# Performance work log

Measured on AMD Instinct MI355X. Metric: run time of the kernel, lower is better.

## Reference

```python
import jax, jax.numpy as jnp
import numpy as np

N_BOND = 2_000_000
N_ATOM = 100_000
N_STRUCT = 2
THREEBODY_CUTOFF = 0.8


def setup_inputs() -> dict:
    key = jax.random.key(0)
    k1, k2 = jax.random.split(key)
    # bonds grouped (sorted) by source atom, as _compute_threebody assumes
    bond_src = jnp.sort(jax.random.randint(k1, (N_BOND,), 0, N_ATOM))
    bond_length = jax.random.uniform(k2, (N_BOND,), dtype=jnp.float32)
    n_atoms = jnp.full((N_STRUCT,), N_ATOM // N_STRUCT, dtype=jnp.int32)
    return {"bond_src": bond_src, "bond_length": bond_length, "n_atoms": n_atoms}


def reference(bond_src, bond_length, n_atoms):
    """Vectorized equivalent of compute_threebody_indices.

    Returns (bond_indices [T,2] pairs of ORIGINAL bond ids, n_triple_ij [n_bond],
    n_triple_i [n_atom], n_triple_s [n_struct]). Replaces the O(n) Python loops
    with segment-sum (degree count), prefix-sum (CSR offsets) and a flat
    enumeration of ordered within-atom bond pairs (j != k).
    """
    n_bond = bond_src.shape[0]
    n_atom = int(jnp.sum(n_atoms))
    n_struct = n_atoms.shape[0]

    # --- filter bonds by three-body cutoff, remember original bond ids ---
    mask = bond_length <= THREEBODY_CUTOFF
    kept = jnp.nonzero(mask)[0]          # original bond indices of surviving bonds
    src = bond_src[kept]                 # still sorted (subset of a sorted array)

    # --- per-atom bond counts and CSR offsets (parallel histogram + scan) ---
    deg = jax.ops.segment_sum(jnp.ones_like(src), src, num_segments=n_atom)
    bond_offset = jnp.cumsum(deg) - deg  # start of each atom's bond block

    # --- triples per atom / per bond / per structure ---
    n_triple_i = deg * (deg - 1)
    T = int(jnp.sum(n_triple_i))

    # --- enumerate all ordered pairs (j, k), j != k, within each atom block ---
    tri_atom = jnp.repeat(jnp.arange(n_atom), n_triple_i, total_repeat_length=T)
    tri_start = (jnp.cumsum(n_triple_i) - n_triple_i)[tri_atom]
    t = jnp.arange(T) - tri_start        # local triple index in [0, d*(d-1))
    d = deg[tri_atom]                    # d >= 2 wherever triples exist
    j = t // (d - 1)
    kp = t % (d - 1)
    k = kp + (kp >= j).astype(kp.dtype)  # skip k == j, preserving loop order
    b0 = bond_offset[tri_atom] + j       # relative (filtered) bond index
    b1 = bond_offset[tri_atom] + k
    bond_indices = jnp.stack([kept[b0], kept[b1]], axis=1)  # back to ORIGINAL ids

    # angles per ORIGINAL bond: deg(src)-1 for surviving bonds, 0 for filtered
    n_triple_ij = jnp.zeros(n_bond, dtype=deg.dtype).at[kept].set(deg[src] - 1)

    # angles per structure
    struct_id = jnp.repeat(jnp.arange(n_struct), n_atoms, total_repeat_length=n_atom)
    n_triple_s = jax.ops.segment_sum(n_triple_i, struct_id, num_segments=n_struct)

    return bond_indices, n_triple_ij, n_triple_i, n_triple_s
```

## Files before the change

### kernel.cpp

```cpp
#include <hip/hip_runtime.h>


#define CUTOFF 0.8f
#define NATOM_C 100000
#define EPB_A 4096
#define EPB_B 1024
#define EPB_IJ 1024
#define TPB2 2048
#define WIN 64

#define ST_AGG (1ull << 32)
#define ST_PFX (2ull << 32)

__device__ __forceinline__ int block_scan_256(int v, int tid, int* sh, int* bsum) {
    sh[tid] = v;
    __syncthreads();
    #pragma unroll
    for (int off = 1; off < 256; off <<= 1) {
        int x = (tid >= off) ? sh[tid - off] : 0;
        __syncthreads();
        sh[tid] += x;
        __syncthreads();
    }
    *bsum = sh[255];
    return sh[tid] - v;
}

__device__ __forceinline__ long long wave_lookback(unsigned long long* status,
                                                   int bid, int bsum, int lane) {
    if (lane == 0)
        __hip_atomic_store(&status[bid],
                           ST_AGG | (unsigned long long)(unsigned)bsum,
                           __ATOMIC_RELEASE, __HIP_MEMORY_SCOPE_AGENT);
    long long excl = 0;
    int w = bid - 1;
    while (w >= 0) {
        int idx = w - lane;
        unsigned long long st;
        if (idx >= 0)
            st = __hip_atomic_load(&status[idx], __ATOMIC_ACQUIRE,
                                   __HIP_MEMORY_SCOPE_AGENT);
        else
            st = ST_PFX;
        unsigned hi = (unsigned)(st >> 32);
        unsigned long long pfx_mask   = __ballot(hi == 2u);
        unsigned long long inval_mask = __ballot(hi != 1u && hi != 2u);
        int first_pfx   = pfx_mask   ? ((int)__ffsll((long long)pfx_mask) - 1)   : 64;
        int first_inval = inval_mask ? ((int)__ffsll((long long)inval_mask) - 1) : 64;
        if (first_inval < first_pfx) continue;
        int val = (lane <= first_pfx) ? (int)(unsigned)st : 0;
        #pragma unroll
        for (int off = 32; off > 0; off >>= 1) val += __shfl_down(val, off, 64);
        val = __shfl(val, 0, 64);
        excl += val;
        if (first_pfx < 64) break;
        w -= 64;
    }
    if (lane == 0)
        __hip_atomic_store(&status[bid],
                           ST_PFX | (unsigned long long)(unsigned)(excl + bsum),
                           __ATOMIC_RELEASE, __HIP_MEMORY_SCOPE_AGENT);
    return excl;
}

__global__ __launch_bounds__(256, 2)
void kA_scan(const float* __restrict__ len, const int* __restrict__ src,
             int* __restrict__ bo, int* __restrict__ ckept,
             unsigned long long* __restrict__ statusA, int n_bond, int n_atom) {
    __shared__ int sh[256];
    __shared__ int sh_last[256];
    __shared__ int sh_bexcl;
    int tid = threadIdx.x;
    int base0 = blockIdx.x * EPB_A + tid * 16;
    int sv[16];
    unsigned mbits = 0;
    #pragma unroll
    for (int g = 0; g < 4; g++) {
        int b = base0 + g * 4;
        if (b + 3 < n_bond) {
            float4 L = *(const float4*)(len + b);
            int4  S = *(const int4*)(src + b);
            sv[g*4+0] = S.x; sv[g*4+1] = S.y; sv[g*4+2] = S.z; sv[g*4+3] = S.w;
            mbits |= (unsigned)(L.x <= CUTOFF) << (g*4+0);
            mbits |= (unsigned)(L.y <= CUTOFF) << (g*4+1);
            mbits |= (unsigned)(L.z <= CUTOFF) << (g*4+2);
            mbits |= (unsigned)(L.w <= CUTOFF) << (g*4+3);
        } else {
            #pragma unroll
            for (int i = 0; i < 4; i++) {
                int idx = b + i;
                bool in = idx < n_bond;
                sv[g*4+i] = in ? src[idx] : 0;
                if (in && len[idx] <= CUTOFF) mbits |= 1u << (g*4+i);
            }
        }
    }
    int s = __popc(mbits);
    sh_last[tid] = sv[15];
    int bsum;
    int texcl = block_scan_256(s, tid, sh, &bsum);
    if (tid < 64) {
        long long e = wave_lookback(statusA, blockIdx.x, bsum, tid);
        if (tid == 0) sh_bexcl = (int)e;
    }
    __syncthreads();
    int run = sh_bexcl + texcl;
    int p;
    if (tid > 0)              p = sh_last[tid - 1];
    else if (blockIdx.x > 0)  p = src[base0 - 1];
    else                      p = -1;
    #pragma unroll
    for (int i = 0; i < 16; i++) {
        int idx = base0 + i;
        if (idx < n_bond) {
            int a = sv[i];
            if (a != p) {
                for (int q = p + 1; q <= a; q++) bo[q] = run;
                p = a;
            }
            if ((mbits >> i) & 1u) { ckept[run] = idx; run++; }
            if (idx == n_bond - 1) {
                for (int q = a + 1; q <= n_atom; q++) bo[q] = run;
            }
        }
    }
}

__global__ __launch_bounds__(256, 2)
void kB_atoms(const int* __restrict__ bo, int* __restrict__ deg,
              int* __restrict__ out_i, int* __restrict__ tstart,
              int* __restrict__ block_atom,
              unsigned long long* __restrict__ statusB, int n_atom) {
    __shared__ int sh[256];
    __shared__ int sh_bexcl;
    int tid = threadIdx.x;
    int base = blockIdx.x * EPB_B + tid * 4;
    int d[4], tr[4];
    if (base + 4 <= n_atom) {
        int4 b4 = *(const int4*)(bo + base);
        int  b5 = bo[base + 4];
        d[0] = b4.y - b4.x; d[1] = b4.z - b4.y; d[2] = b4.w - b4.z; d[3] = b5 - b4.w;
    } else {
        #pragma unroll
        for (int i = 0; i < 4; i++) {
            int a = base + i;
            d[i] = (a < n_atom) ? (bo[a + 1] - bo[a]) : 0;
        }
    }
    int ssum = 0;
    #pragma unroll
    for (int i = 0; i < 4; i++) { tr[i] = d[i] * (d[i] - 1); ssum += tr[i]; }
    #pragma unroll
    for (int i = 0; i < 4; i++) {
        int a = base + i;
        if (a < n_atom) { deg[a] = d[i]; out_i[a] = tr[i]; }
    }
    int bsum;
    int texcl = block_scan_256(ssum, tid, sh, &bsum);
    if (tid < 64) {
        long long e = wave_lookback(statusB, blockIdx.x, bsum, tid);
        if (tid == 0) sh_bexcl = (int)e;
    }
    __syncthreads();
    int run = sh_bexcl + texcl;
    #pragma unroll
    for (int i = 0; i < 4; i++) {
        int a = base + i;
        if (a < n_atom) {
            tstart[a] = run;
            int ts1 = run + tr[i];
            for (int b2 = (run + TPB2 - 1) / TPB2; b2 * TPB2 < ts1; b2++)
                block_atom[b2] = a;
            run = ts1;
            if (a == n_atom - 1) tstart[n_atom] = run;
        }
    }
}

__device__ __forceinline__ void triple_pair(int tp, int dm1, int bof,
                                            const int* __restrict__ ckept,
                                            int& x, int& y) {
    float r = 1.0f / (float)dm1;
    int j = (int)((float)tp * r);
    int rem = tp - j * dm1;
    if (rem < 0)         { j -= 1; rem += dm1; }
    else if (rem >= dm1) { j += 1; rem -= dm1; }
    int k = rem + ((rem >= j) ? 1 : 0);
    x = ckept[bof + j];
    y = ckept[bof + k];
}

__global__ void kCT(const float* __restrict__ len, const int* __restrict__ src,
                    const int* __restrict__ deg, const int* __restrict__ bo,
                    const int* __restrict__ tstart, const int* __restrict__ ckept,
                    const int* __restrict__ block_atom,
                    const int* __restrict__ n_atoms_arr,
                    int4* __restrict__ out4, int* __restrict__ out_ij,
                    int* __restrict__ out_s,
                    int n_bond, int n_atom, int n_struct, int T,
                    int nblkIJ, int nblkT) {
    int tid = threadIdx.x;
    if ((int)blockIdx.x < nblkIJ) {
        int base = blockIdx.x * EPB_IJ + tid * 4;
        if (base + 3 < n_bond) {
            float4 L = *(const float4*)(len + base);
            int4  S = *(const int4*)(src + base);
            int4 r;
            r.x = (L.x <= CUTOFF) ? (deg[S.x] - 1) : 0;
            r.y = (L.y <= CUTOFF) ? (deg[S.y] - 1) : 0;
            r.z = (L.z <= CUTOFF) ? (deg[S.z] - 1) : 0;
            r.w = (L.w <= CUTOFF) ? (deg[S.w] - 1) : 0;
            *(int4*)(out_ij + base) = r;
        } else {
            for (int i = 0; i < 4; i++) {
                int idx = base + i;
                if (idx < n_bond)
                    out_ij[idx] = (len[idx] <= CUTOFF) ? (deg[src[idx]] - 1) : 0;
            }
        }
    }
    if (blockIdx.x == 0 && tid == 0) {
        int off = 0;
        for (int s2 = 0; s2 < n_struct; s2++) {
            int c = n_atoms_arr[s2];
            out_s[s2] = tstart[off + c] - tstart[off];
            off += c;
        }
    }
    if ((int)blockIdx.x >= nblkT) return;
    __shared__ int s_ts[WIN + 1];
    __shared__ int s_bo[WIN];
    __shared__ int s_dm1[WIN];
    int a0 = block_atom[blockIdx.x];
    for (int i = tid; i <= WIN; i += 256) {
        int ai = a0 + i; if (ai > n_atom) ai = n_atom;
        s_ts[i] = tstart[ai];
    }
    for (int i = tid; i < WIN; i += 256) {
        int ai = a0 + i; if (ai >= n_atom) ai = n_atom - 1;
        s_bo[i]  = bo[ai];
        s_dm1[i] = deg[ai] - 1;
    }
    __syncthreads();
    int a_off = 0;
    #pragma unroll
    for (int it = 0; it < TPB2 / 512; it++) {
        int t0 = blockIdx.x * TPB2 + it * 512 + tid * 2;
        if (t0 >= T) return;
        while (a_off < WIN && t0 >= s_ts[a_off + 1]) a_off++;
        int x0, y0, x1, y1;
        if (a_off < WIN) {
            triple_pair(t0 - s_ts[a_off], s_dm1[a_off], s_bo[a_off], ckept, x0, y0);
        } else {
            int a = a0 + WIN;
            while (a + 1 <= n_atom && t0 >= tstart[a + 1]) a++;
            triple_pair(t0 - tstart[a], deg[a] - 1, bo[a], ckept, x0, y0);
        }
        int a1 = a_off;
        while (a1 < WIN && t0 + 1 >= s_ts[a1 + 1]) a1++;
        if (a1 < WIN) {
            triple_pair(t0 + 1 - s_ts[a1], s_dm1[a1], s_bo[a1], ckept, x1, y1);
        } else {
            int a = a0 + WIN;
            while (a + 1 <= n_atom && t0 + 1 >= tstart[a + 1]) a++;
            triple_pair(t0 + 1 - tstart[a], deg[a] - 1, bo[a], ckept, x1, y1);
        }
        out4[t0 >> 1] = make_int4(x0, y0, x1, y1);
    }
}

extern "C" void kernel_launch(void* const* d_in, const int* in_sizes, int n_in,
                              void* d_out, int out_size, void* d_ws, size_t ws_size,
                              hipStream_t stream) {
    const int*   bond_src    = (const int*)d_in[0];
    const float* bond_len    = (const float*)d_in[1];
    const int*   n_atoms_arr = (const int*)d_in[2];
    int n_bond   = in_sizes[0];
    int n_struct = in_sizes[2];
    const int n_atom = NATOM_C;
    int T2 = out_size - n_bond - n_atom - n_struct;
    int T  = T2 / 2;

    int nblkA  = (n_bond + EPB_A - 1) / EPB_A;
    int nblkB  = (n_atom + EPB_B - 1) / EPB_B;
    int nblkIJ = (n_bond + EPB_IJ - 1) / EPB_IJ;
    int nblkT  = (T + TPB2 - 1) / TPB2;
    int nblkG  = nblkIJ > nblkT ? nblkIJ : nblkT;

    char* w = (char*)d_ws;
    unsigned long long* statusA = (unsigned long long*)w;  w += (size_t)nblkA * 8;
    unsigned long long* statusB = (unsigned long long*)w;  w += (size_t)nblkB * 8;
    w = (char*)(((size_t)w + 15) & ~(size_t)15);
    int* bo         = (int*)w;  w += (size_t)(n_atom + 1) * 4;
    int* deg        = (int*)w;  w += (size_t)n_atom * 4;
    int* tstart     = (int*)w;  w += (size_t)(n_atom + 1) * 4;
    int* block_atom = (int*)w;  w += (size_t)(nblkT > 0 ? nblkT : 1) * 4;
    int* ckept      = (int*)w;  w += (size_t)n_bond * 4;

    int*  out       = (int*)d_out;
    int4* out4      = (int4*)out;
    int*  out_ij    = out + T2;
    int*  out_i     = out_ij + n_bond;
    int*  out_s     = out_i + n_atom;

    kA_scan <<<nblkA, 256, 0, stream>>>(bond_len, bond_src, bo, ckept, statusA,
                                        n_bond, n_atom);
    kB_atoms<<<nblkB, 256, 0, stream>>>(bo, deg, out_i, tstart, block_atom,
                                        statusB, n_atom);
    kCT     <<<nblkG, 256, 0, stream>>>(bond_len, bond_src, deg, bo, tstart, ckept,
                                        block_atom, n_atoms_arr, out4, out_ij, out_s,
                                        n_bond, n_atom, n_struct, T, nblkIJ, nblkT);
}
```

Before: 296.3 us.

## Stage kept-bond ids in LDS for triples and move n_triple_ij into atom kernel

The per-bond n_triple_ij pass moves out of the triples kernel into the atom-scan kernel as a grid-stride loop, and the deg array is dropped in favour of differences of bond offsets. The triples kernel now handles larger tiles (8192 triples, 128-atom window) and stages each block's contiguous slice of kept-bond ids into shared memory, falling back to global loads when the span exceeds capacity. This aims to cut redundant global gathers of ckept and to even out the work split between kernels. It costs more LDS per block, which may lower occupancy, and there are fewer, larger triple blocks.

```diff
diff --git a/kernel.cpp b/kernel.cpp
--- a/kernel.cpp
+++ b/kernel.cpp
@@ -5,9 +5,9 @@
 #define NATOM_C 100000
 #define EPB_A 4096
 #define EPB_B 1024
-#define EPB_IJ 1024
-#define TPB2 2048
-#define WIN 64
+#define TPB2 8192
+#define WIN 128
+#define CKCAP 6144
 
 #define ST_AGG (1ull << 32)
 #define ST_PFX (2ull << 32)
@@ -127,98 +127,102 @@
 }
 
 __global__ __launch_bounds__(256, 2)
-void kB_atoms(const int* __restrict__ bo, int* __restrict__ deg,
-              int* __restrict__ out_i, int* __restrict__ tstart,
-              int* __restrict__ block_atom,
-              unsigned long long* __restrict__ statusB, int n_atom) {
+void kB_atoms(const float* __restrict__ len, const int* __restrict__ src,
+              const int* __restrict__ bo, int* __restrict__ out_i,
+              int* __restrict__ tstart, int* __restrict__ block_atom,
+              int* __restrict__ out_ij,
+              unsigned long long* __restrict__ statusB,
+              int n_bond, int n_atom, int nScan) {
     __shared__ int sh[256];
     __shared__ int sh_bexcl;
     int tid = threadIdx.x;
-    int base = blockIdx.x * EPB_B + tid * 4;
-    int d[4], tr[4];
-    if (base + 4 <= n_atom) {
-        int4 b4 = *(const int4*)(bo + base);
-        int  b5 = bo[base + 4];
-        d[0] = b4.y - b4.x; d[1] = b4.z - b4.y; d[2] = b4.w - b4.z; d[3] = b5 - b4.w;
-    } else {
+    if ((int)blockIdx.x < nScan) {
+        int base = blockIdx.x * EPB_B + tid * 4;
+        int d[4], tr[4];
+        if (base + 4 <= n_atom) {
+            int4 b4 = *(const int4*)(bo + base);
+            int  b5 = bo[base + 4];
+            d[0] = b4.y - b4.x; d[1] = b4.z - b4.y; d[2] = b4.w - b4.z; d[3] = b5 - b4.w;
+        } else {
+            #pragma unroll
+            for (int i = 0; i < 4; i++) {
+                int a = base + i;
+                d[i] = (a < n_atom) ? (bo[a + 1] - bo[a]) : 0;
+            }
+        }
+        int ssum = 0;
+        #pragma unroll
+        for (int i = 0; i < 4; i++) { tr[i] = d[i] * (d[i] - 1); ssum += tr[i]; }
         #pragma unroll
         for (int i = 0; i < 4; i++) {
             int a = base + i;
-            d[i] = (a < n_atom) ? (bo[a + 1] - bo[a]) : 0;
-        }
-    }
-    int ssum = 0;
-    #pragma unroll
-    for (int i = 0; i < 4; i++) { tr[i] = d[i] * (d[i] - 1); ssum += tr[i]; }
-    #pragma unroll
-    for (int i = 0; i < 4; i++) {
-        int a = base + i;
-        if (a < n_atom) { deg[a] = d[i]; out_i[a] = tr[i]; }
-    }
-    int bsum;
-    int texcl = block_scan_256(ssum, tid, sh, &bsum);
-    if (tid < 64) {
-        long long e = wave_lookback(statusB, blockIdx.x, bsum, tid);
-        if (tid == 0) sh_bexcl = (int)e;
-    }
-    __syncthreads();
-    int run = sh_bexcl + texcl;
-    #pragma unroll
-    for (int i = 0; i < 4; i++) {
-        int a = base + i;
-        if (a < n_atom) {
-            tstart[a] = run;
-            int ts1 = run + tr[i];
-            for (int b2 = (run + TPB2 - 1) / TPB2; b2 * TPB2 < ts1; b2++)
-                block_atom[b2] = a;
-            run = ts1;
-            if (a == n_atom - 1) tstart[n_atom] = run;
-        }
-    }
-}
-
-__device__ __forceinline__ void triple_pair(int tp, int dm1, int bof,
-                                            const int* __restrict__ ckept,
-                                            int& x, int& y) {
+            if (a < n_atom) out_i[a] = tr[i];
+        }
+        int bsum;
+        int texcl = block_scan_256(ssum, tid, sh, &bsum);
+        if (tid < 64) {
+            long long e = wave_lookback(statusB, blockIdx.x, bsum, tid);
+            if (tid == 0) sh_bexcl = (int)e;
+        }
+        __syncthreads();
+        int run = sh_bexcl + texcl;
+        #pragma unroll
+        for (int i = 0; i < 4; i++) {
+            int a = base + i;
+            if (a < n_atom) {
+                tstart[a] = run;
+                int ts1 = run + tr[i];
+                for (int b2 = (run + TPB2 - 1) / TPB2; b2 * TPB2 < ts1; b2++)
+                    block_atom[b2] = a;
+                run = ts1;
+                if (a == n_atom - 1) tstart[n_atom] = run;
+            }
+        }
+    }
+    int nq = (n_bond + 3) >> 2;
+    int stride = gridDim.x * 256;
+    for (int q = blockIdx.x * 256 + tid; q < nq; q += stride) {
+        int b = q * 4;
+        if (b + 3 < n_bond) {
+            float4 L = *(const float4*)(len + b);
+            int4  S = *(const int4*)(src + b);
+            int4 r;
+            r.x = (L.x <= CUTOFF) ? (bo[S.x + 1] - bo[S.x] - 1) : 0;
+            r.y = (L.y <= CUTOFF) ? (bo[S.y + 1] - bo[S.y] - 1) : 0;
+            r.z = (L.z <= CUTOFF) ? (bo[S.z + 1] - bo[S.z] - 1) : 0;
+            r.w = (L.w <= CUTOFF) ? (bo[S.w + 1] - bo[S.w] - 1) : 0;
+            *(int4*)(out_ij + b) = r;
+        } else {
+            for (int i = 0; i < 4; i++) {
+                int idx = b + i;
+                if (idx < n_bond) {
+                    int sa = src[idx];
+                    out_ij[idx] = (len[idx] <= CUTOFF) ? (bo[sa + 1] - bo[sa] - 1) : 0;
+                }
+            }
+        }
+    }
+}
+
+__device__ __forceinline__ void div_fix(int tp, int dm1, int& j, int& k) {
     float r = 1.0f / (float)dm1;
-    int j = (int)((float)tp * r);
+    j = (int)((float)tp * r);
     int rem = tp - j * dm1;
     if (rem < 0)         { j -= 1; rem += dm1; }
     else if (rem >= dm1) { j += 1; rem -= dm1; }
-    int k = rem + ((rem >= j) ? 1 : 0);
-    x = ckept[bof + j];
-    y = ckept[bof + k];
-}
-
-__global__ void kCT(const float* __restrict__ len, const int* __restrict__ src,
-                    const int* __restrict__ deg, const int* __restrict__ bo,
-                    const int* __restrict__ tstart, const int* __restrict__ ckept,
-                    const int* __restrict__ block_atom,
-                    const int* __restrict__ n_atoms_arr,
-                    int4* __restrict__ out4, int* __restrict__ out_ij,
-                    int* __restrict__ out_s,
-                    int n_bond, int n_atom, int n_struct, int T,
-                    int nblkIJ, int nblkT) {
+    k = rem + ((rem >= j) ? 1 : 0);
+}
+
+__global__ __launch_bounds__(256, 4)
+void kT_triples(const int* __restrict__ tstart, const int* __restrict__ bo,
+                const int* __restrict__ ckept, const int* __restrict__ block_atom,
+                const int* __restrict__ n_atoms_arr,
+                int4* __restrict__ out4, int* __restrict__ out_s,
+                int n_atom, int n_struct, int T) {
+    __shared__ int s_ts[WIN + 1];
+    __shared__ int s_bo[WIN + 1];
+    __shared__ int s_ck[CKCAP];
     int tid = threadIdx.x;
-    if ((int)blockIdx.x < nblkIJ) {
-        int base = blockIdx.x * EPB_IJ + tid * 4;
-        if (base + 3 < n_bond) {
-            float4 L = *(const float4*)(len + base);
-            int4  S = *(const int4*)(src + base);
-            int4 r;
-            r.x = (L.x <= CUTOFF) ? (deg[S.x] - 1) : 0;
-            r.y = (L.y <= CUTOFF) ? (deg[S.y] - 1) : 0;
-            r.z = (L.z <= CUTOFF) ? (deg[S.z] - 1) : 0;
-            r.w = (L.w <= CUTOFF) ? (deg[S.w] - 1) : 0;
-            *(int4*)(out_ij + base) = r;
-        } else {
-            for (int i = 0; i < 4; i++) {
-                int idx = base + i;
-                if (idx < n_bond)
-                    out_ij[idx] = (len[idx] <= CUTOFF) ? (deg[src[idx]] - 1) : 0;
-            }
-        }
-    }
     if (blockIdx.x == 0 && tid == 0) {
         int off = 0;
         for (int s2 = 0; s2 < n_struct; s2++) {
@@ -227,20 +231,19 @@
             off += c;
         }
     }
-    if ((int)blockIdx.x >= nblkT) return;
-    __shared__ int s_ts[WIN + 1];
-    __shared__ int s_bo[WIN];
-    __shared__ int s_dm1[WIN];
+    if (T <= 0) return;
     int a0 = block_atom[blockIdx.x];
     for (int i = tid; i <= WIN; i += 256) {
         int ai = a0 + i; if (ai > n_atom) ai = n_atom;
         s_ts[i] = tstart[ai];
-    }
-    for (int i = tid; i < WIN; i += 256) {
-        int ai = a0 + i; if (ai >= n_atom) ai = n_atom - 1;
-        s_bo[i]  = bo[ai];
-        s_dm1[i] = deg[ai] - 1;
-    }
+        s_bo[i] = bo[ai];
+    }
+    __syncthreads();
+    int kbase = s_bo[0];
+    int span  = s_bo[WIN] - kbase;
+    bool staged = (span <= CKCAP);
+    if (staged)
+        for (int i = tid; i < span; i += 256) s_ck[i] = ckept[kbase + i];
     __syncthreads();
     int a_off = 0;
     #pragma unroll
@@ -250,20 +253,30 @@
         while (a_off < WIN && t0 >= s_ts[a_off + 1]) a_off++;
         int x0, y0, x1, y1;
         if (a_off < WIN) {
-            triple_pair(t0 - s_ts[a_off], s_dm1[a_off], s_bo[a_off], ckept, x0, y0);
+            int dm1 = s_bo[a_off + 1] - s_bo[a_off] - 1;
+            int lof = s_bo[a_off] - kbase;
+            int j, k; div_fix(t0 - s_ts[a_off], dm1, j, k);
+            if (staged) { x0 = s_ck[lof + j]; y0 = s_ck[lof + k]; }
+            else        { x0 = ckept[kbase + lof + j]; y0 = ckept[kbase + lof + k]; }
         } else {
             int a = a0 + WIN;
             while (a + 1 <= n_atom && t0 >= tstart[a + 1]) a++;
-            triple_pair(t0 - tstart[a], deg[a] - 1, bo[a], ckept, x0, y0);
+            int j, k; div_fix(t0 - tstart[a], bo[a + 1] - bo[a] - 1, j, k);
+            x0 = ckept[bo[a] + j]; y0 = ckept[bo[a] + k];
         }
         int a1 = a_off;
         while (a1 < WIN && t0 + 1 >= s_ts[a1 + 1]) a1++;
         if (a1 < WIN) {
-            triple_pair(t0 + 1 - s_ts[a1], s_dm1[a1], s_bo[a1], ckept, x1, y1);
+            int dm1 = s_bo[a1 + 1] - s_bo[a1] - 1;
+            int lof = s_bo[a1] - kbase;
+            int j, k; div_fix(t0 + 1 - s_ts[a1], dm1, j, k);
+            if (staged) { x1 = s_ck[lof + j]; y1 = s_ck[lof + k]; }
+            else        { x1 = ckept[kbase + lof + j]; y1 = ckept[kbase + lof + k]; }
         } else {
             int a = a0 + WIN;
             while (a + 1 <= n_atom && t0 + 1 >= tstart[a + 1]) a++;
-            triple_pair(t0 + 1 - tstart[a], deg[a] - 1, bo[a], ckept, x1, y1);
+            int j, k; div_fix(t0 + 1 - tstart[a], bo[a + 1] - bo[a] - 1, j, k);
+            x1 = ckept[bo[a] + j]; y1 = ckept[bo[a] + k];
         }
         out4[t0 >> 1] = make_int4(x0, y0, x1, y1);
     }
@@ -281,20 +294,20 @@
     int T2 = out_size - n_bond - n_atom - n_struct;
     int T  = T2 / 2;
 
-    int nblkA  = (n_bond + EPB_A - 1) / EPB_A;
-    int nblkB  = (n_atom + EPB_B - 1) / EPB_B;
-    int nblkIJ = (n_bond + EPB_IJ - 1) / EPB_IJ;
-    int nblkT  = (T + TPB2 - 1) / TPB2;
-    int nblkG  = nblkIJ > nblkT ? nblkIJ : nblkT;
+    int nblkA = (n_bond + EPB_A - 1) / EPB_A;
+    int nScan = (n_atom + EPB_B - 1) / EPB_B;
+    int nblkB = 488;
+    if (nblkB < nScan) nblkB = nScan;
+    int nblkT = (T + TPB2 - 1) / TPB2;
+    if (nblkT < 1) nblkT = 1;
 
     char* w = (char*)d_ws;
     unsigned long long* statusA = (unsigned long long*)w;  w += (size_t)nblkA * 8;
-    unsigned long long* statusB = (unsigned long long*)w;  w += (size_t)nblkB * 8;
+    unsigned long long* statusB = (unsigned long long*)w;  w += (size_t)nScan * 8;
     w = (char*)(((size_t)w + 15) & ~(size_t)15);
-    int* bo         = (int*)w;  w += (size_t)(n_atom + 1) * 4;
-    int* deg        = (int*)w;  w += (size_t)n_atom * 4;
+    int* bo         = (int*)w;  w += (size_t)(n_atom + 4) * 4;
     int* tstart     = (int*)w;  w += (size_t)(n_atom + 1) * 4;
-    int* block_atom = (int*)w;  w += (size_t)(nblkT > 0 ? nblkT : 1) * 4;
+    int* block_atom = (int*)w;  w += (size_t)nblkT * 4;
     int* ckept      = (int*)w;  w += (size_t)n_bond * 4;
 
     int*  out       = (int*)d_out;
@@ -303,11 +316,12 @@
     int*  out_i     = out_ij + n_bond;
     int*  out_s     = out_i + n_atom;
 
-    kA_scan <<<nblkA, 256, 0, stream>>>(bond_len, bond_src, bo, ckept, statusA,
-                                        n_bond, n_atom);
-    kB_atoms<<<nblkB, 256, 0, stream>>>(bo, deg, out_i, tstart, block_atom,
-                                        statusB, n_atom);
-    kCT     <<<nblkG, 256, 0, stream>>>(bond_len, bond_src, deg, bo, tstart, ckept,
-                                        block_atom, n_atoms_arr, out4, out_ij, out_s,
-                                        n_bond, n_atom, n_struct, T, nblkIJ, nblkT);
-}
+    kA_scan   <<<nblkA, 256, 0, stream>>>(bond_len, bond_src, bo, ckept, statusA,
+                                          n_bond, n_atom);
+    kB_atoms  <<<nblkB, 256, 0, stream>>>(bond_len, bond_src, bo, out_i, tstart,
+                                          block_atom, out_ij, statusB,
+                                          n_bond, n_atom, nScan);
+    kT_triples<<<nblkT, 256, 0, stream>>>(tstart, bo, ckept, block_atom,
+                                          n_atoms_arr, out4, out_s,
+                                          n_atom, n_struct, T);
+}
```

Result: slower. 307.2 us (+3.7%).
